# Kernel tuning notes

Measured on AMD Instinct MI355X. Metric: run time of the kernel, lower is better.

## Reference

```python
import jax, jax.numpy as jnp
import numpy as np

TOP_P = 0.9  # forward default arg, fixed to exercise the top-p path


def setup_inputs() -> dict:
    key = jax.random.key(0)
    k1, k2 = jax.random.split(key)
    B, V = 128, 128000
    logits = jax.random.normal(k1, (B, V), dtype=jnp.float32) * 2.0
    # temperatures in [0.5, 1.5) to avoid divide-by-near-zero
    temperatures = jax.random.uniform(k2, (B,), dtype=jnp.float32, minval=0.5, maxval=1.5)
    return {"logits": logits, "temperatures": temperatures, "top_k": 50}


def reference(logits, temperatures, top_k):
    B, V = logits.shape
    neg_inf = jnp.float32(-jnp.inf)

    # temperature scale + softmax
    scaled = logits.astype(jnp.float32) / temperatures[:, None]
    probs = jax.nn.softmax(scaled, axis=-1)  # (B, V)

    brow = jnp.arange(B)[:, None]

    # top-k filter: keep top-k probs, fill rest with -inf (matches torch scatter into full(-inf))
    if top_k > 0:
        k = min(top_k, V)
        vals, idx = jax.lax.top_k(probs, k)  # (B, k)
        probs = jnp.full_like(probs, neg_inf).at[brow, idx].set(vals)

    # top-p (nucleus) filter: sort desc, cumsum, mask tail beyond top_p (always keep first)
    if TOP_P < 1.0:
        order = jnp.argsort(-probs, axis=-1)              # descending order indices (-inf sorts last)
        sorted_probs = jnp.take_along_axis(probs, order, axis=-1)
        cum = jnp.cumsum(sorted_probs, axis=-1)
        remove = cum > TOP_P
        remove = remove.at[:, 0].set(False)
        sorted_probs = jnp.where(remove, neg_inf, sorted_probs)
        probs = probs.at[brow, order].set(sorted_probs)   # scatter back to original positions

    # Gumbel-max-style sampling: argmax(probs / Exp(1) noise), noise clamped to >= 1e-10
    kn = jax.random.fold_in(jax.random.key(0), 1)
    noise = jnp.maximum(jax.random.exponential(kn, probs.shape, dtype=jnp.float32), 1e-10)
    return jnp.argmax(probs / noise, axis=-1)  # (B,) int tokens
```

## Files before the change

### kernel.cpp

```cpp
#include <hip/hip_runtime.h>
#include <stdint.h>
#include <limits.h>

#define THREEFRY_PARTITIONABLE 1

#define NTK   512
#define NWAVE (NTK/64)
#define NBUCK 4096
#define BPT   (NBUCK/NTK)
#define CAPS  256
#define CAPG  2048
#define CAPF  512
#define KMAX  512
#define SMAX  32
#define CHUNK_TARGET 32768

#define NT1   1024
#define CAP1  4096

#if __has_builtin(__builtin_amdgcn_exp2f)
#define FAST_EXP2(x) __builtin_amdgcn_exp2f(x)
#else
#define FAST_EXP2(x) exp2f(x)
#endif

__device__ __forceinline__ uint32_t rotl32(uint32_t v, int r) {
  return (v << r) | (v >> (32 - r));
}
__device__ __forceinline__ void tfround(uint32_t& x0, uint32_t& x1, int r) {
  x0 += x1; x1 = rotl32(x1, r); x1 ^= x0;
}
__device__ __forceinline__ void threefry2x32(uint32_t k0, uint32_t k1,
                                             uint32_t x0, uint32_t x1,
                                             uint32_t& o0, uint32_t& o1) {
  uint32_t k2 = k0 ^ k1 ^ 0x1BD11BDAu;
  x0 += k0; x1 += k1;
  tfround(x0,x1,13); tfround(x0,x1,15); tfround(x0,x1,26); tfround(x0,x1,6);
  x0 += k1; x1 += k2 + 1u;
  tfround(x0,x1,17); tfround(x0,x1,29); tfround(x0,x1,16); tfround(x0,x1,24);
  x0 += k2; x1 += k0 + 2u;
  tfround(x0,x1,13); tfround(x0,x1,15); tfround(x0,x1,26); tfround(x0,x1,6);
  x0 += k0; x1 += k1 + 3u;
  tfround(x0,x1,17); tfround(x0,x1,29); tfround(x0,x1,16); tfround(x0,x1,24);
  x0 += k1; x1 += k2 + 4u;
  tfround(x0,x1,13); tfround(x0,x1,15); tfround(x0,x1,26); tfround(x0,x1,6);
  x0 += k2; x1 += k0 + 5u;
  o0 = x0; o1 = x1;
}
__device__ __forceinline__ float jax_noise(uint32_t kn0, uint32_t kn1,
                                           unsigned long long i,
                                           unsigned long long total) {
  uint32_t o0, o1, bits;
#if THREEFRY_PARTITIONABLE
  threefry2x32(kn0, kn1, (uint32_t)(i >> 32), (uint32_t)(i & 0xFFFFFFFFull), o0, o1);
  bits = o0 ^ o1;
#else
  unsigned long long H = total >> 1;
  if (i < H) { threefry2x32(kn0, kn1, (uint32_t)i, (uint32_t)(i + H), o0, o1); bits = o0; }
  else       { threefry2x32(kn0, kn1, (uint32_t)(i - H), (uint32_t)i, o0, o1); bits = o1; }
#endif
  float u = __uint_as_float((bits >> 9) | 0x3f800000u) - 1.0f;
  float e = -log1pf(-u);
  return fmaxf(e, 1e-10f);
}
__device__ __forceinline__ uint32_t fkey(float f) {
  uint32_t u = __float_as_uint(f);
  return u ^ ((u >> 31) ? 0xFFFFFFFFu : 0x80000000u);
}
__device__ __forceinline__ float unfkey_floor(uint32_t keyT) {
  if (keyT == 0u) return -INFINITY;
  return __uint_as_float((keyT & 0x80000000u) ? (keyT ^ 0x80000000u) : ~keyT);
}
__device__ __forceinline__ int clamp_k(int k) {
  if (k < 1) k = 1;
  if (k > KMAX) k = KMAX;
  return k;
}

__device__ __forceinline__ void block_kth_bucket(uint32_t* hist, uint32_t* wtot,
                                                 int* beta_sh, int k,
                                                 int tid, int lane, int wave) {
  const int base = tid * BPT;
  uint32_t tsum = 0;
#pragma unroll
  for (int j = 0; j < BPT; j++) tsum += hist[base + j];
  uint32_t incl = tsum;
  for (int off = 1; off < 64; off <<= 1) {
    uint32_t v = __shfl_down(incl, off);
    if (lane + off < 64) incl += v;
  }
  if (lane == 0) wtot[wave] = incl;
  __syncthreads();
  uint32_t above = incl - tsum;
  for (int w = wave + 1; w < NWAVE; w++) above += wtot[w];
  if (above < (uint32_t)k && above + tsum >= (uint32_t)k) {
    uint32_t run = above;
    for (int j = BPT - 1; j >= 0; j--) {
      run += hist[base + j];
      if (run >= (uint32_t)k) { *beta_sh = base + j; break; }
    }
  }
  __syncthreads();
}

__global__ __launch_bounds__(NTK)
void sampler_stream(const float* __restrict__ logits,
                    const float* __restrict__ temps,
                    const int* __restrict__ topk_ptr,
                    float* __restrict__ msArr,
                    double* __restrict__ dsumArr,
                    int* __restrict__ cntArr,
                    float2* __restrict__ pairs,
                    int B, int V, int S, int chunk) {
  const int blk = blockIdx.x;
  const int b = blk / S, sp = blk % S;
  const int tid = threadIdx.x, lane = tid & 63, wave = tid >> 6;

  __shared__ uint32_t hist[NBUCK];
  __shared__ float wm[NWAVE];
  __shared__ double wsum[NWAVE];
  __shared__ uint32_t wtot[NWAVE];
  __shared__ int beta_sh, cnum_sh;

  if (tid == 0) { beta_sh = 0; cnum_sh = 0; }
  for (int i = tid; i < NBUCK; i += NTK) hist[i] = 0;

  const float T = temps[b];
  const float cf = (float)(1.4426950408889634 / (double)T);
  const int k = clamp_k(*topk_ptr);

  const int start = sp * chunk;
  const int end = min(start + chunk, V);
  const float* row = logits + (size_t)b * (size_t)V;
  const int n = end - start;
  const int n4 = n >> 2;
  const float4* row4 = (const float4*)(row + start);

  float tmax = -INFINITY;
  float acc0 = 0.f, acc1 = 0.f;
  for (int i = tid; i < n4; i += NTK) {
    float4 f = row4[i];
    tmax = fmaxf(tmax, fmaxf(fmaxf(f.x, f.y), fmaxf(f.z, f.w)));
    acc0 += FAST_EXP2(f.x * cf) + FAST_EXP2(f.z * cf);
    acc1 += FAST_EXP2(f.y * cf) + FAST_EXP2(f.w * cf);
  }
  for (int v = start + n4 * 4 + tid; v < end; v += NTK) {
    float f = row[v];
    tmax = fmaxf(tmax, f);
    acc0 += FAST_EXP2(f * cf);
  }

  float bm = tmax;
  for (int off = 32; off; off >>= 1)
    bm = fmaxf(bm, __shfl_down(bm, off));
  if (lane == 0) wm[wave] = bm;

  double ds = (double)acc0 + (double)acc1;
  for (int off = 32; off; off >>= 1)
    ds += __shfl_down(ds, off);
  if (lane == 0) wsum[wave] = ds;

  if (tmax != -INFINITY) atomicAdd(&hist[fkey(tmax) >> 20], 1u);
  __syncthreads();

  if (tid == 0) {
    float m_sp = wm[0];
#pragma unroll
    for (int w = 1; w < NWAVE; w++) m_sp = fmaxf(m_sp, wm[w]);
    msArr[blk] = m_sp;
    double t = 0.0;
    for (int w = 0; w < NWAVE; w++) t += wsum[w];
    dsumArr[blk] = t;
  }

  block_kth_bucket(hist, wtot, &beta_sh, k, tid, lane, wave);

  const float fT = unfkey_floor((uint32_t)beta_sh << 20);
  float2* myp = pairs + (size_t)blk * CAPS;

  if (tmax >= fT) {
    for (int i = tid; i < n4; i += NTK) {
      float4 f = row4[i];
      const int vb = start + i * 4;
      if (f.x >= fT) { int p = atomicAdd(&cnum_sh, 1); if (p < CAPS) myp[p] = make_float2(f.x, __int_as_float(vb)); }
      if (f.y >= fT) { int p = atomicAdd(&cnum_sh, 1); if (p < CAPS) myp[p] = make_float2(f.y, __int_as_float(vb + 1)); }
      if (f.z >= fT) { int p = atomicAdd(&cnum_sh, 1); if (p < CAPS) myp[p] = make_float2(f.z, __int_as_float(vb + 2)); }
      if (f.w >= fT) { int p = atomicAdd(&cnum_sh, 1); if (p < CAPS) myp[p] = make_float2(f.w, __int_as_float(vb + 3)); }
    }
    for (int v = start + n4 * 4 + tid; v < end; v += NTK) {
      float f = row[v];
      if (f >= fT) { int p = atomicAdd(&cnum_sh, 1); if (p < CAPS) myp[p] = make_float2(f, __int_as_float(v)); }
    }
  }
  __syncthreads();
  if (tid == 0) cntArr[blk] = min(cnum_sh, CAPS);
}

__global__ __launch_bounds__(NTK)
void sampler_finalize(const float* __restrict__ temps,
                      const int* __restrict__ topk_ptr,
                      const float* __restrict__ msArr,
                      const double* __restrict__ dsumArr,
                      const int* __restrict__ cntArr,
                      const float2* __restrict__ pairs,
                      int* __restrict__ out,
                      int B, int V, int S) {
  const int b = blockIdx.x;
  const int tid = threadIdx.x, lane = tid & 63, wave = tid >> 6;

  __shared__ uint32_t hist[NBUCK];
  __shared__ float gv[CAPG];
  __shared__ int   gi[CAPG];
  __shared__ float c2v[CAPF];
  __shared__ int   c2i[CAPF];
  __shared__ float c2p[CAPF];
  __shared__ float sv[KMAX];
  __shared__ int   si[KMAX];
  __shared__ float sc[KMAX];
  __shared__ int   offL[SMAX + 1];
  __shared__ int   cnL[SMAX];
  __shared__ float msL[SMAX];
  __shared__ double dsL[SMAX];
  __shared__ uint32_t wtot[NWAVE];
  __shared__ int beta_sh, cnt2_sh, L_sh;
  __shared__ float m_sh, D_sh;

  const int k = clamp_k(*topk_ptr);
  const float T = temps[b];

  if (tid == 0) { beta_sh = 0; cnt2_sh = 0; }
  if (tid < S) {
    msL[tid] = msArr[b * S + tid];
    dsL[tid] = dsumArr[b * S + tid];
    int c = cntArr[b * S + tid];
    cnL[tid] = (c < CAPS) ? c : CAPS;
  }
  for (int i = tid; i < NBUCK; i += NTK) hist[i] = 0;
  __syncthreads();

  if (tid == 0) {
    int acc = 0;
    for (int j = 0; j < S; j++) { offL[j] = acc; acc += cnL[j]; }
    offL[S] = acc;
  }

  if (wave == 1 || (NWAVE == 1 && wave == 0)) {
    float msp = (lane < S) ? msL[lane] : -INFINITY;
    float mg = msp;
    for (int off = 32; off; off >>= 1)
      mg = fmaxf(mg, __shfl_down(mg, off));
    mg = __shfl(mg, 0);
    double term = (lane < S) ? dsL[lane] : 0.0;
    for (int off = 32; off; off >>= 1)
      term += __shfl_down(term, off);
    if (lane == 0) {
      const double cd = 1.4426950408889634 / (double)T;
      D_sh = (float)(term * exp2(-(double)mg * cd));
      m_sh = mg / T;
    }
  }
  __syncthreads();

  const int TC = min(offL[S], CAPG);

  for (int t = tid; t < TC; t += NTK) {
    int j = 0;
#pragma unroll
    for (int jj = 1; jj <= SMAX; jj++)
      if (jj <= S) j += (t >= offL[jj]);
    float2 pr = pairs[(size_t)(b * S + j) * CAPS + (t - offL[j])];
    gv[t] = pr.x;
    gi[t] = __float_as_int(pr.y);
    atomicAdd(&hist[fkey(pr.x) >> 20], 1u);
  }
  __syncthreads();

  block_kth_bucket(hist, wtot, &beta_sh, k, tid, lane, wave);

  const float fT = unfkey_floor((uint32_t)beta_sh << 20);
  for (int t = tid; t < TC; t += NTK) {
    float val = gv[t];
    if (val >= fT) {
      int pos = atomicAdd(&cnt2_sh, 1);
      if (pos < CAPF) { c2v[pos] = val; c2i[pos] = gi[t]; }
    }
  }
  __syncthreads();

  const int C = min(cnt2_sh, CAPF);
  const float m = m_sh, D = D_sh;
  for (int i = tid; i < C; i += NTK)
    c2p[i] = expf(c2v[i] / T - m) / D;
  __syncthreads();

  for (int i = tid; i < C; i += NTK) {
    float pi = c2p[i];
    int   ii = c2i[i];
    int r = 0;
    for (int j = 0; j < C; j++) {
      float pj = c2p[j];
      r += (pj > pi) || (pj == pi && c2i[j] < ii);
    }
    if (r < k) { sv[r] = pi; si[r] = ii; }
  }
  __syncthreads();

  const int kk = (k < C) ? k : C;
  if (tid == 0) {
    float cum = 0.f;
    int L = 1;
    for (int j = 0; j < kk; j++) {
      cum += sv[j];
      if (j == 0) continue;
      if (cum <= 0.9f) L = j + 1; else break;
    }
    L_sh = L;
  }
  __syncthreads();

  const int L = L_sh;
  {
    uint32_t kn0, kn1;
    threefry2x32(0u, 0u, 0u, 1u, kn0, kn1);
    unsigned long long total = (unsigned long long)B * (unsigned long long)V;
    for (int j = tid; j < L; j += NTK) {
      unsigned long long flat = (unsigned long long)b * (unsigned long long)V
                              + (unsigned long long)si[j];
      sc[j] = sv[j] / jax_noise(kn0, kn1, flat, total);
    }
  }
  __syncthreads();

  if (tid == 0) {
    float bs = -1.0f;
    int   bi = INT_MAX;
    for (int j = 0; j < L; j++) {
      if (sc[j] > bs || (sc[j] == bs && si[j] < bi)) { bs = sc[j]; bi = si[j]; }
    }
    out[b] = bi;
  }
}

__global__ __launch_bounds__(NT1, 1)
void sampler_fallback(const float* __restrict__ logits,
                      const float* __restrict__ temps,
                      const int* __restrict__ topk_ptr,
                      int* __restrict__ out,
                      int B, int V) {
  const int b    = blockIdx.x;
  const int tid  = threadIdx.x;
  const int lane = tid & 63;
  const int wave = tid >> 6;

  __shared__ uint32_t hist[NBUCK];
  __shared__ float    cand_p[CAP1];
  __shared__ int      cand_i[CAP1];
  __shared__ float    wmax[16];
  __shared__ double   wsum[16];
  __shared__ float    svals[KMAX];
  __shared__ int      sidx[KMAX];
  __shared__ float    m_sh, D_sh;
  __shared__ int      beta_sh, cnum_sh, L_sh;

  const float T = temps[b];
  const float* row = logits + (size_t)b * (size_t)V;
  int k = clamp_k(*topk_ptr);
  if (k > V) k = V;

  if (tid == 0) { beta_sh = 1; cnum_sh = 0; }
  for (int i = tid; i < NBUCK; i += NT1) hist[i] = 0;
  __syncthreads();

  float t8[8];
#pragma unroll
  for (int j = 0; j < 8; j++) t8[j] = -INFINITY;
  float mymax = -INFINITY;
  for (int v = tid; v < V; v += NT1) {
    float s = row[v] / T;
    mymax = fmaxf(mymax, s);
    if (s > t8[0]) {
      t8[0] = s;
#pragma unroll
      for (int j = 1; j < 8; j++)
        if (t8[j-1] > t8[j]) { float tmp = t8[j]; t8[j] = t8[j-1]; t8[j-1] = tmp; }
    }
  }
  for (int off = 32; off > 0; off >>= 1)
    mymax = fmaxf(mymax, __shfl_down(mymax, off));
  if (lane == 0) wmax[wave] = mymax;
#pragma unroll
  for (int j = 0; j < 8; j++)
    if (t8[j] != -INFINITY) atomicAdd(&hist[fkey(t8[j]) >> 20], 1u);
  __syncthreads();
  if (tid == 0) {
    float m = -INFINITY;
    for (int w = 0; w < 16; w++) m = fmaxf(m, wmax[w]);
    m_sh = m;
  }
  if (wave == 1) {
    int base = lane * 64;
    uint32_t ssum = 0;
    for (int j = 0; j < 64; j++) ssum += hist[base + ((j + lane) & 63)];
    uint32_t incl = ssum;
    for (int off = 1; off < 64; off <<= 1) {
      uint32_t vv = __shfl_down(incl, off);
      if (lane + off < 64) incl += vv;
    }
    uint32_t higher = incl - ssum;
    if (higher < (uint32_t)k && incl >= (uint32_t)k) {
      uint32_t run = higher;
      for (int j = 63; j >= 0; j--) {
        run += hist[base + j];
        if (run >= (uint32_t)k) { beta_sh = base + j; break; }
      }
    }
  }
  __syncthreads();
  const float m = m_sh;
  const uint32_t keyT = (uint32_t)((beta_sh >= 1 ? beta_sh - 1 : 0)) << 20;
  double dsum = 0.0;
  for (int v = tid; v < V; v += NT1) {
    float s = row[v] / T;
    float e = expf(s - m);
    dsum += (double)e;
    if (fkey(s) >= keyT) {
      int pos = atomicAdd(&cnum_sh, 1);
      if (pos < CAP1) { cand_p[pos] = e; cand_i[pos] = v; }
    }
  }
  for (int off = 32; off > 0; off >>= 1)
    dsum += __shfl_down(dsum, off);
  if (lane == 0) wsum[wave] = dsum;
  __syncthreads();
  if (tid == 0) {
    double t = 0.0;
    for (int w = 0; w < 16; w++) t += wsum[w];
    D_sh = (float)t;
  }
  __syncthreads();
  const float D = D_sh;
  const int C = (cnum_sh < CAP1) ? cnum_sh : CAP1;
  for (int i = tid; i < C; i += NT1) cand_p[i] = cand_p[i] / D;
  __syncthreads();
  for (int i = tid; i < C; i += NT1) {
    float pi = cand_p[i];
    int   ii = cand_i[i];
    int r = 0;
    for (int j = 0; j < C; j++) {
      float pj = cand_p[j];
      r += (pj > pi) || (pj == pi && cand_i[j] < ii);
    }
    if (r < k) { svals[r] = pi; sidx[r] = ii; }
  }
  __syncthreads();
  if (tid == 0) {
    float cum = 0.f;
    int L = 1;
    for (int j = 0; j < k; j++) {
      cum += svals[j];
      if (j == 0) continue;
      if (cum <= 0.9f) L = j + 1; else break;
    }
    L_sh = L;
  }
  __syncthreads();
  const int L = L_sh;
  if (tid < L) {
    uint32_t kn0, kn1;
    threefry2x32(0u, 0u, 0u, 1u, kn0, kn1);
    unsigned long long total = (unsigned long long)B * (unsigned long long)V;
    unsigned long long flat = (unsigned long long)b * (unsigned long long)V
                            + (unsigned long long)sidx[tid];
    cand_p[tid] = svals[tid] / jax_noise(kn0, kn1, flat, total);
  }
  __syncthreads();
  if (tid == 0) {
    float bs = -1.0f;
    int   bi = INT_MAX;
    for (int j = 0; j < L; j++) {
      if (cand_p[j] > bs || (cand_p[j] == bs && sidx[j] < bi)) { bs = cand_p[j]; bi = sidx[j]; }
    }
    out[b] = bi;
  }
}

extern "C" void kernel_launch(void* const* d_in, const int* in_sizes, int n_in,
                              void* d_out, int out_size, void* d_ws, size_t ws_size,
                              hipStream_t stream) {
  const float* logits = (const float*)d_in[0];
  const float* temps  = (const float*)d_in[1];
  const int*   topk   = (const int*)d_in[2];
  int* out = (int*)d_out;

  int B = in_sizes[1];
  int V = in_sizes[0] / B;

  int S = (V + CHUNK_TARGET - 1) / CHUNK_TARGET;
  if (S > SMAX) S = SMAX;
  if (S < 1) S = 1;
  size_t need;
  for (;;) {
    need = (size_t)B * S * (sizeof(double) + sizeof(float) + sizeof(int))
         + (size_t)B * S * CAPS * sizeof(float2);
    if (need <= ws_size || S <= 2) break;
    S >>= 1;
  }

  if (ws_size < need || S < 2) {
    sampler_fallback<<<dim3(B), dim3(NT1), 0, stream>>>(logits, temps, topk, out, B, V);
    return;
  }

  int chunk = (((V + S - 1) / S) + 3) & ~3;

  double* dsumArr = (double*)d_ws;
  float*  msArr   = (float*)(dsumArr + (size_t)B * S);
  int*    cntArr  = (int*)(msArr + (size_t)B * S);
  float2* pairs   = (float2*)(cntArr + (size_t)B * S);

  sampler_stream<<<dim3(B * S), dim3(NTK), 0, stream>>>(
      logits, temps, topk, msArr, dsumArr, cntArr, pairs, B, V, S, chunk);
  sampler_finalize<<<dim3(B), dim3(NTK), 0, stream>>>(
      temps, topk, msArr, dsumArr, cntArr, pairs, out, B, V, S);
}
```

Baseline: 127.6 us.

## Track per-thread top-2 to skip candidate rescans and halve chunk size

Each thread now tracks its two largest logits with their indices instead of only the max. If only the top value passes the threshold, it is emitted directly without re-reading the chunk. The main loop is unrolled four ways with independent loads, and the chunk target is halved so more blocks split each row. The cost is extra compare/select work per element and more partial results for the finalize kernel to merge.

```diff
diff --git a/kernel.cpp b/kernel.cpp
--- a/kernel.cpp
+++ b/kernel.cpp
@@ -13,7 +13,7 @@
 #define CAPF  512
 #define KMAX  512
 #define SMAX  32
-#define CHUNK_TARGET 32768
+#define CHUNK_TARGET 16384
 
 #define NT1   1024
 #define CAP1  4096
@@ -132,25 +132,51 @@
   const int start = sp * chunk;
   const int end = min(start + chunk, V);
   const float* row = logits + (size_t)b * (size_t)V;
-  const int n = end - start;
+  const int n = (end > start) ? (end - start) : 0;
   const int n4 = n >> 2;
   const float4* row4 = (const float4*)(row + start);
 
-  float tmax = -INFINITY;
+  float v0 = -INFINITY, v1 = -INFINITY;
+  int   i0 = 0, i1 = 0;
   float acc0 = 0.f, acc1 = 0.f;
-  for (int i = tid; i < n4; i += NTK) {
-    float4 f = row4[i];
-    tmax = fmaxf(tmax, fmaxf(fmaxf(f.x, f.y), fmaxf(f.z, f.w)));
+
+  auto proc = [&](float f, int idx) {
+    bool gt0 = f > v0;
+    bool gt1 = f > v1;
+    float nv1 = gt0 ? v0 : (gt1 ? f : v1);
+    int   ni1 = gt0 ? i0 : (gt1 ? idx : i1);
+    v1 = nv1; i1 = ni1;
+    v0 = gt0 ? f : v0;
+    i0 = gt0 ? idx : i0;
+  };
+  auto proc4 = [&](float4 f, int vb) {
+    proc(f.x, vb); proc(f.y, vb + 1); proc(f.z, vb + 2); proc(f.w, vb + 3);
     acc0 += FAST_EXP2(f.x * cf) + FAST_EXP2(f.z * cf);
     acc1 += FAST_EXP2(f.y * cf) + FAST_EXP2(f.w * cf);
+  };
+
+  int i = tid;
+  for (; i + 3 * NTK < n4; i += 4 * NTK) {
+    float4 fa = row4[i];
+    float4 fb = row4[i + NTK];
+    float4 fc = row4[i + 2 * NTK];
+    float4 fd = row4[i + 3 * NTK];
+    proc4(fa, start + i * 4);
+    proc4(fb, start + (i + NTK) * 4);
+    proc4(fc, start + (i + 2 * NTK) * 4);
+    proc4(fd, start + (i + 3 * NTK) * 4);
+  }
+  for (; i < n4; i += NTK) {
+    float4 fa = row4[i];
+    proc4(fa, start + i * 4);
   }
   for (int v = start + n4 * 4 + tid; v < end; v += NTK) {
     float f = row[v];
-    tmax = fmaxf(tmax, f);
+    proc(f, v);
     acc0 += FAST_EXP2(f * cf);
   }
 
-  float bm = tmax;
+  float bm = v0;
   for (int off = 32; off; off >>= 1)
     bm = fmaxf(bm, __shfl_down(bm, off));
   if (lane == 0) wm[wave] = bm;
@@ -160,7 +186,7 @@
     ds += __shfl_down(ds, off);
   if (lane == 0) wsum[wave] = ds;
 
-  if (tmax != -INFINITY) atomicAdd(&hist[fkey(tmax) >> 20], 1u);
+  if (v0 != -INFINITY) atomicAdd(&hist[fkey(v0) >> 20], 1u);
   __syncthreads();
 
   if (tid == 0) {
@@ -178,18 +204,23 @@
   const float fT = unfkey_floor((uint32_t)beta_sh << 20);
   float2* myp = pairs + (size_t)blk * CAPS;
 
-  if (tmax >= fT) {
-    for (int i = tid; i < n4; i += NTK) {
-      float4 f = row4[i];
-      const int vb = start + i * 4;
-      if (f.x >= fT) { int p = atomicAdd(&cnum_sh, 1); if (p < CAPS) myp[p] = make_float2(f.x, __int_as_float(vb)); }
-      if (f.y >= fT) { int p = atomicAdd(&cnum_sh, 1); if (p < CAPS) myp[p] = make_float2(f.y, __int_as_float(vb + 1)); }
-      if (f.z >= fT) { int p = atomicAdd(&cnum_sh, 1); if (p < CAPS) myp[p] = make_float2(f.z, __int_as_float(vb + 2)); }
-      if (f.w >= fT) { int p = atomicAdd(&cnum_sh, 1); if (p < CAPS) myp[p] = make_float2(f.w, __int_as_float(vb + 3)); }
-    }
-    for (int v = start + n4 * 4 + tid; v < end; v += NTK) {
-      float f = row[v];
-      if (f >= fT) { int p = atomicAdd(&cnum_sh, 1); if (p < CAPS) myp[p] = make_float2(f, __int_as_float(v)); }
+  if (v0 >= fT) {
+    if (v1 >= fT) {
+      for (int i2 = tid; i2 < n4; i2 += NTK) {
+        float4 f = row4[i2];
+        const int vb = start + i2 * 4;
+        if (f.x >= fT) { int p = atomicAdd(&cnum_sh, 1); if (p < CAPS) myp[p] = make_float2(f.x, __int_as_float(vb)); }
+        if (f.y >= fT) { int p = atomicAdd(&cnum_sh, 1); if (p < CAPS) myp[p] = make_float2(f.y, __int_as_float(vb + 1)); }
+        if (f.z >= fT) { int p = atomicAdd(&cnum_sh, 1); if (p < CAPS) myp[p] = make_float2(f.z, __int_as_float(vb + 2)); }
+        if (f.w >= fT) { int p = atomicAdd(&cnum_sh, 1); if (p < CAPS) myp[p] = make_float2(f.w, __int_as_float(vb + 3)); }
+      }
+      for (int v = start + n4 * 4 + tid; v < end; v += NTK) {
+        float f = row[v];
+        if (f >= fT) { int p = atomicAdd(&cnum_sh, 1); if (p < CAPS) myp[p] = make_float2(f, __int_as_float(v)); }
+      }
+    } else {
+      int p = atomicAdd(&cnum_sh, 1);
+      if (p < CAPS) myp[p] = make_float2(v0, __int_as_float(i0));
     }
   }
   __syncthreads();
```

Measured after the change: 118.9 us. 1.07x faster.
